# Optimization experiments

Measured on AMD Instinct MI355X. Metric: run time of the kernel, lower is better.

## Reference

```python
import jax, jax.numpy as jnp
import numpy as np

EPS = 1e-12


def conv3(x, W, b):
    # x: [B,C,H,W], W: [O,I,3,3] -> SAME conv, stride 1
    y = jax.lax.conv_general_dilated(x, W, (1, 1), 'SAME',
                                     dimension_numbers=('NCHW', 'OIHW', 'NCHW'))
    return y + b[None, :, None, None]


def unfold3(x):
    # torch F.unfold(kernel=3, padding=1): [B,C,H,W] -> [B, C*9, H*W]
    B, C, H, W = x.shape
    xp = jnp.pad(x, ((0, 0), (0, 0), (1, 1), (1, 1)))
    patches = jnp.stack([xp[:, :, i:i + H, j:j + W]
                         for i in range(3) for j in range(3)], axis=2)  # [B,C,9,H,W]
    return patches.reshape(B, C * 9, H * W)


def fold3(u, H, W):
    # torch F.fold(kernel=3, padding=1): [B, C*9, H*W] -> [B,C,H,W] (overlap-add)
    B = u.shape[0]
    C = u.shape[1] // 9
    p = u.reshape(B, C, 3, 3, H, W)
    out = jnp.zeros((B, C, H + 2, W + 2), u.dtype)
    for i in range(3):
        for j in range(3):
            out = out.at[:, :, i:i + H, j:j + W].add(p[:, :, i, j])
    return out[:, :, 1:-1, 1:-1]


def l2norm(v, axis):
    n = jnp.sqrt(jnp.sum(v * v, axis=axis, keepdims=True))
    return v / jnp.maximum(n, EPS)


def setup_inputs() -> dict:
    key = jax.random.key(0)
    ks = jax.random.split(key, 10)
    in_c, q_c = 64, 32
    B, H, W = 1, 96, 96
    s = 0.05
    return {
        'x':  jax.random.normal(ks[0], (B, in_c, H, W), jnp.float32),
        'W1': jax.random.normal(ks[1], (in_c, in_c, 3, 3), jnp.float32) * s,
        'b1': jax.random.normal(ks[2], (in_c,), jnp.float32) * s,
        'W2': jax.random.normal(ks[3], (in_c, in_c, 3, 3), jnp.float32) * s,
        'b2': jax.random.normal(ks[4], (in_c,), jnp.float32) * s,
        'Wq': jax.random.normal(ks[5], (q_c, in_c, 3, 3), jnp.float32) * s,
        'bq': jax.random.normal(ks[6], (q_c,), jnp.float32) * s,
        'Wk': jax.random.normal(ks[7], (q_c, in_c, 3, 3), jnp.float32) * s,
        'bk': jax.random.normal(ks[8], (q_c,), jnp.float32) * s,
    }


def reference(x, W1, b1, W2, b2, Wq, bq, Wk, bk):
    TOPK = 5
    B, C, H, W = x.shape
    L = H * W

    feature = jax.nn.relu(conv3(jax.nn.relu(conv3(x, W1, b1)), W2, b2))
    q = conv3(x, Wq, bq)
    k = conv3(x, Wk, bk)

    q_unfold = l2norm(unfold3(q), axis=1)                      # [B, Q9, L]
    k_unfold = l2norm(jnp.swapaxes(unfold3(k), 1, 2), axis=2)  # [B, L, Q9]

    R_qk = jnp.einsum('blc,bcm->blm', k_unfold, q_unfold)      # [B, L_k, L_q]

    # topk over dim=1 (key positions) for each query position
    vals, idxs = jax.lax.top_k(jnp.swapaxes(R_qk, 1, 2), TOPK)  # [B, L_q, K]
    R_maxs = jnp.swapaxes(vals, 1, 2)                           # [B, K, L]
    R_indexs = jnp.swapaxes(idxs, 1, 2)                         # [B, K, L]

    x_unfold = unfold3(x)                                       # [B, C*9, L]
    acc = jnp.zeros_like(x)
    for i in range(1, TOPK):
        idx = R_indexs[:, i, :][:, None, :]                     # [B,1,L]
        T_unfold = jnp.take_along_axis(x_unfold, idx, axis=2)   # [B, C*9, L]
        T = fold3(T_unfold, H, W) / 9.0
        S = R_maxs[:, i, :].reshape(B, 1, H, W)
        acc = acc + T * S
    y = feature + x + acc / float(TOPK - 1)
    return y
```

## Files before the change

### kernel.cpp

```cpp
#include <hip/hip_runtime.h>
#include <math.h>

#define HH 96
#define WW 96
#define LL 9216
#define PW 98
#define PCH (PW * PW)
#define D9 288
#define TOPK 5
#define NK 6
#define NCAND 8
#define KSPLIT 32
#define CPQ (KSPLIT * NK)
#define KEYS_PER_SPLIT (LL / KSPLIT)
#define PASSES (KEYS_PER_SPLIT / 32)
#define CHUNKS (32 * 36)
#define KROW 292

typedef short short8 __attribute__((ext_vector_type(8)));
typedef float f32x16 __attribute__((ext_vector_type(16)));

__device__ __forceinline__ float  asf(unsigned u) { union { unsigned u; float f; } a; a.u = u; return a.f; }
__device__ __forceinline__ unsigned asu(float f)  { union { float f; unsigned u; } a; a.f = f; return a.u; }

__device__ __forceinline__ unsigned short f2bf(float f) {
    unsigned u = asu(f);
    unsigned r = u + 0x7fff + ((u >> 16) & 1);
    return (unsigned short)(r >> 16);
}

template<int N>
__device__ __forceinline__ void ins_med3(float* v, float x) {
    float nv[N];
    nv[0] = fmaxf(v[0], x);
    #pragma unroll
    for (int s = 1; s < N; ++s) nv[s] = __builtin_amdgcn_fmed3f(v[s-1], v[s], x);
    #pragma unroll
    for (int s = 0; s < N; ++s) v[s] = nv[s];
}

__device__ __forceinline__ bool better_tb(float av, int ai, float bv, int bi) {
    return (av > bv) || (av == bv && ai < bi);
}

template<int N>
__device__ __forceinline__ void insert_tb(float (&v)[N], int (&ix)[N], float nv, int ni) {
    if (better_tb(nv, ni, v[N-1], ix[N-1])) {
        v[N-1] = nv; ix[N-1] = ni;
        #pragma unroll
        for (int s = N-1; s > 0; --s) {
            if (better_tb(v[s], ix[s], v[s-1], ix[s-1])) {
                float tv = v[s]; v[s] = v[s-1]; v[s-1] = tv;
                int ti = ix[s]; ix[s] = ix[s-1]; ix[s-1] = ti;
            }
        }
    }
}

__global__ __launch_bounds__(256) void pad_init_kernel(
    const float* __restrict__ x, float* __restrict__ xpad, float* __restrict__ c1pad)
{
    int e = blockIdx.x * 256 + threadIdx.x;
    if (blockIdx.y == 1) { c1pad[e] = 0.0f; return; }
    int c = e / PCH, rem = e - c * PCH;
    int r = rem / PW, col = rem - r * PW;
    float val = 0.0f;
    if ((unsigned)(r - 1) < 96u && (unsigned)(col - 1) < 96u)
        val = x[(size_t)c * LL + (r - 1) * WW + (col - 1)];
    xpad[e] = val;
}

template<int NCO>
__device__ __forceinline__ void conv_pipe(
    const float* __restrict__ inpad, const float* __restrict__ Wt,
    const float* __restrict__ bias, int co0,
    float (&acc)[NCO][2])
{
    int t = blockIdx.x * 256 + threadIdx.x;
    int pix0 = t * 2;
    int y = pix0 / WW, x0 = pix0 - y * WW;
    const float* base = inpad + y * PW + x0;

    #pragma unroll
    for (int j = 0; j < NCO; ++j) acc[j][0] = acc[j][1] = bias[co0 + j];

    float2 A[3][2], B[3][2];
    #pragma unroll
    for (int u = 0; u < 3; ++u) {
        A[u][0] = *(const float2*)(base + u * PW);
        A[u][1] = *(const float2*)(base + u * PW + 2);
    }

    #pragma unroll 1
    for (int ci = 0; ci < 64; ci += 2) {
        const float* nb = base + (size_t)(ci + 1) * PCH;
        #pragma unroll
        for (int u = 0; u < 3; ++u) {
            B[u][0] = *(const float2*)(nb + u * PW);
            B[u][1] = *(const float2*)(nb + u * PW + 2);
        }
        {
            const float* wb = Wt + ((size_t)co0 * 64 + ci) * 9;
            #pragma unroll
            for (int j = 0; j < NCO; ++j) {
                const float* wp = wb + (size_t)j * 64 * 9;
                #pragma unroll
                for (int u = 0; u < 3; ++u) {
                    float r0 = A[u][0].x, r1 = A[u][0].y, r2 = A[u][1].x, r3 = A[u][1].y;
                    float w0 = wp[u*3], w1 = wp[u*3+1], w2 = wp[u*3+2];
                    acc[j][0] = fmaf(r0, w0, acc[j][0]);
                    acc[j][1] = fmaf(r1, w0, acc[j][1]);
                    acc[j][0] = fmaf(r1, w1, acc[j][0]);
                    acc[j][1] = fmaf(r2, w1, acc[j][1]);
                    acc[j][0] = fmaf(r2, w2, acc[j][0]);
                    acc[j][1] = fmaf(r3, w2, acc[j][1]);
                }
            }
        }
        if (ci + 2 < 64) {
            const float* nb2 = base + (size_t)(ci + 2) * PCH;
            #pragma unroll
            for (int u = 0; u < 3; ++u) {
                A[u][0] = *(const float2*)(nb2 + u * PW);
                A[u][1] = *(const float2*)(nb2 + u * PW + 2);
            }
        }
        {
            const float* wb = Wt + ((size_t)co0 * 64 + (ci + 1)) * 9;
            #pragma unroll
            for (int j = 0; j < NCO; ++j) {
                const float* wp = wb + (size_t)j * 64 * 9;
                #pragma unroll
                for (int u = 0; u < 3; ++u) {
                    float r0 = B[u][0].x, r1 = B[u][0].y, r2 = B[u][1].x, r3 = B[u][1].y;
                    float w0 = wp[u*3], w1 = wp[u*3+1], w2 = wp[u*3+2];
                    acc[j][0] = fmaf(r0, w0, acc[j][0]);
                    acc[j][1] = fmaf(r1, w0, acc[j][1]);
                    acc[j][0] = fmaf(r1, w1, acc[j][0]);
                    acc[j][1] = fmaf(r2, w1, acc[j][1]);
                    acc[j][0] = fmaf(r2, w2, acc[j][0]);
                    acc[j][1] = fmaf(r3, w2, acc[j][1]);
                }
            }
        }
    }
}

__global__ __launch_bounds__(256) void conv_stage1_kernel(
    const float* __restrict__ xpad,
    const float* __restrict__ W1, const float* __restrict__ b1, float* __restrict__ c1pad,
    const float* __restrict__ Wq, const float* __restrict__ bq,
    const float* __restrict__ Wk, const float* __restrict__ bk,
    float* __restrict__ qq, float* __restrict__ kk)
{
    int g = blockIdx.y;
    int pix0 = (blockIdx.x * 256 + threadIdx.x) * 2;
    int y = pix0 / WW, x0 = pix0 - y * WW;

    if (g < 16) {
        float acc[4][2];
        conv_pipe<4>(xpad, W1, b1, g * 4, acc);
        #pragma unroll
        for (int j = 0; j < 4; ++j) {
            float* o = c1pad + (size_t)(g * 4 + j) * PCH + (y + 1) * PW + (x0 + 1);
            o[0] = fmaxf(acc[j][0], 0.0f);
            o[1] = fmaxf(acc[j][1], 0.0f);
        }
    } else if (g < 24) {
        float acc[4][2];
        conv_pipe<4>(xpad, Wq, bq, (g - 16) * 4, acc);
        #pragma unroll
        for (int j = 0; j < 4; ++j)
            *(float2*)(qq + (size_t)((g - 16) * 4 + j) * LL + pix0) = make_float2(acc[j][0], acc[j][1]);
    } else {
        float acc[4][2];
        conv_pipe<4>(xpad, Wk, bk, (g - 24) * 4, acc);
        #pragma unroll
        for (int j = 0; j < 4; ++j)
            *(float2*)(kk + (size_t)((g - 24) * 4 + j) * LL + pix0) = make_float2(acc[j][0], acc[j][1]);
    }
}

__global__ __launch_bounds__(256) void conv2_kernel(
    const float* __restrict__ c1pad, const float* __restrict__ W2,
    const float* __restrict__ b2, float* __restrict__ feat)
{
    int pix0 = (blockIdx.x * 256 + threadIdx.x) * 2;
    float acc[2][2];
    conv_pipe<2>(c1pad, W2, b2, blockIdx.y * 2, acc);
    #pragma unroll
    for (int j = 0; j < 2; ++j) {
        float2 o;
        o.x = fmaxf(acc[j][0], 0.0f);
        o.y = fmaxf(acc[j][1], 0.0f);
        *(float2*)(feat + (size_t)(blockIdx.y * 2 + j) * LL + pix0) = o;
    }
}

__global__ __launch_bounds__(256) void transpose_x_kernel(
    const float* __restrict__ x, float* __restrict__ xT)
{
    __shared__ float t[64][65];
    int pix0 = blockIdx.x * 64;
    int lp = threadIdx.x & 63, cg = threadIdx.x >> 6;
    #pragma unroll
    for (int cc = 0; cc < 16; ++cc) {
        int c = cg * 16 + cc;
        t[c][lp] = x[(size_t)c * LL + pix0 + lp];
    }
    __syncthreads();
    #pragma unroll
    for (int pp = 0; pp < 16; ++pp) {
        int pl = cg * 16 + pp;
        xT[(size_t)(pix0 + pl) * 64 + lp] = t[lp][pl];
    }
}

__global__ __launch_bounds__(256) void unfold_norm_kernel(
    const float* __restrict__ qq, float* __restrict__ q_f32, unsigned short* __restrict__ q_bf,
    const float* __restrict__ kk, float* __restrict__ k_f32, unsigned short* __restrict__ k_bf)
{
    const float* in; float* o32; unsigned short* obf;
    if (blockIdx.y == 0) { in = qq; o32 = q_f32; obf = q_bf; }
    else                 { in = kk; o32 = k_f32; obf = k_bf; }

    __shared__ float tile[3][32][34];
    __shared__ float inv_s[32];
    int tid = threadIdx.x;
    int l0 = blockIdx.x * 32;
    int y = l0 / WW, xb = l0 % WW;

    #pragma unroll
    for (int j = 0; j < 13; ++j) {
        int f = j * 256 + tid;
        if (f < 3 * 32 * 34) {
            int col = f % 34, cc = (f / 34) & 31, r = f / (34 * 32);
            int yy = y + r - 1, xv = xb + col - 1;
            float val = ((unsigned)yy < 96u && (unsigned)xv < 96u)
                        ? in[(size_t)cc * LL + yy * 96 + xv] : 0.0f;
            tile[r][cc][col] = val;
        }
    }
    __syncthreads();

    {
        int pxl = tid >> 3, sub = tid & 7;
        float ss = 0.0f;
        #pragma unroll
        for (int cc = 0; cc < 4; ++cc) {
            int c = sub * 4 + cc;
            #pragma unroll
            for (int u = 0; u < 3; ++u)
                #pragma unroll
                for (int v = 0; v < 3; ++v) {
                    float val = tile[u][c][pxl + v];
                    ss = fmaf(val, val, ss);
                }
        }
        ss += __shfl_xor(ss, 1);
        ss += __shfl_xor(ss, 2);
        ss += __shfl_xor(ss, 4);
        if (sub == 0) inv_s[pxl] = 1.0f / fmaxf(sqrtf(ss), 1e-12f);
    }
    __syncthreads();

    #pragma unroll 1
    for (int it = 0; it < 9; ++it) {
        int e = it * 256 + tid;
        int pxl = e / 72, dc = e - pxl * 72;
        int l = l0 + pxl;
        float inv = inv_s[pxl];
        float4 o; float* op = &o.x;
        #pragma unroll
        for (int i = 0; i < 4; ++i) {
            int d = dc * 4 + i;
            int c = d / 9, rm = d - c * 9;
            int u = rm / 3, v = rm - u * 3;
            op[i] = tile[u][c][pxl + v] * inv;
        }
        *(float4*)(o32 + (size_t)l * D9 + dc * 4) = o;
        unsigned short b4[4];
        #pragma unroll
        for (int i = 0; i < 4; ++i) b4[i] = f2bf(op[i]);
        *(uint2*)(obf + (size_t)l * D9 + dc * 4) = *(uint2*)b4;
    }
}

__global__ __launch_bounds__(256, 3) void topk_mfma_kernel(
    const unsigned short* __restrict__ qn_bf, const unsigned short* __restrict__ kn_bf,
    float* __restrict__ valsQ)
{
    __shared__ unsigned short ks[2][32 * KROW];

    int tid  = threadIdx.x;
    int lane = tid & 63;
    int col = lane & 31, khalf = lane >> 5;
    int qtile = blockIdx.x >> 5;
    int split = blockIdx.x & 31;
    int q0w = qtile * 128 + (tid >> 6) * 32;
    int key0 = split * KEYS_PER_SPLIT;

    short8 qf[18];
    {
        const unsigned short* qrow = qn_bf + (size_t)(q0w + col) * D9 + khalf * 8;
        #pragma unroll
        for (int dg = 0; dg < 18; ++dg)
            qf[dg] = *(const short8*)(qrow + dg * 16);
    }

    float lv[NK];
    #pragma unroll
    for (int s = 0; s < NK; ++s) lv[s] = -INFINITY;

    const char* kg = (const char*)kn_bf;
    uint4 pre[5];

    #pragma unroll
    for (int c0 = 0; c0 < 5; ++c0) {
        int c = tid + c0 * 256;
        if (c < CHUNKS) {
            int key = c / 36, off = c - key * 36;
            pre[c0] = *(const uint4*)(kg + (size_t)(key0 + key) * 576 + off * 16);
        }
    }
    #pragma unroll
    for (int c0 = 0; c0 < 5; ++c0) {
        int c = tid + c0 * 256;
        if (c < CHUNKS) {
            int key = c / 36, off = c - key * 36;
            char* d = (char*)ks[0] + key * (KROW*2) + off * 16;
            *(uint2*)d       = *(uint2*)&pre[c0];
            *(uint2*)(d + 8) = *((uint2*)&pre[c0] + 1);
        }
    }
    __syncthreads();

    for (int p = 0; p < PASSES; ++p) {
        if (p + 1 < PASSES) {
            #pragma unroll
            for (int c0 = 0; c0 < 5; ++c0) {
                int c = tid + c0 * 256;
                if (c < CHUNKS) {
                    int key = c / 36, off = c - key * 36;
                    pre[c0] = *(const uint4*)(kg + (size_t)(key0 + (p+1)*32 + key) * 576 + off * 16);
                }
            }
        }

        f32x16 acc = {};
        const char* kb = (const char*)ks[p & 1] + (size_t)col * (KROW*2) + khalf * 16;
        #pragma unroll
        for (int dg = 0; dg < 18; ++dg) {
            short8 af;
            *(uint2*)&af       = *(const uint2*)(kb + dg * 32);
            *((uint2*)&af + 1) = *(const uint2*)(kb + dg * 32 + 8);
            acc = __builtin_amdgcn_mfma_f32_32x32x16_bf16(af, qf[dg], acc, 0, 0, 0);
        }

        int lbase = p * 32 + 4 * khalf;
        #pragma unroll
        for (int r = 0; r < 16; ++r) {
            unsigned lkey = (unsigned)(lbase + (r & 3) + 8 * (r >> 2));
            ins_med3<NK>(lv, asf((asu(acc[r]) & 0xFFFFFE00u) | lkey));
        }

        if (p + 1 < PASSES) {
            #pragma unroll
            for (int c0 = 0; c0 < 5; ++c0) {
                int c = tid + c0 * 256;
                if (c < CHUNKS) {
                    int key = c / 36, off = c - key * 36;
                    char* d = (char*)ks[(p+1) & 1] + key * (KROW*2) + off * 16;
                    *(uint2*)d       = *(uint2*)&pre[c0];
                    *(uint2*)(d + 8) = *((uint2*)&pre[c0] + 1);
                }
            }
        }
        __syncthreads();
    }

    {
        float pv[NK];
        #pragma unroll
        for (int s = 0; s < NK; ++s) pv[s] = __shfl_xor(lv[s], 32);
        #pragma unroll
        for (int s = 0; s < NK; ++s) ins_med3<NK>(lv, pv[s]);
        if (lane < 32) {
            int q = q0w + col;
            float* vq = valsQ + (size_t)q * CPQ + split * NK;
            #pragma unroll
            for (int s = 0; s < NK; ++s) vq[s] = lv[s];
        }
    }
}

__global__ __launch_bounds__(256) void rerank_kernel(
    const float* __restrict__ valsQ,
    const float* __restrict__ qn_f32, const float* __restrict__ kn_f32,
    float* __restrict__ vals, int* __restrict__ idxs)
{
    int tid = threadIdx.x;
    int lane = tid & 63;
    int half = lane >> 5, l32 = lane & 31;
    int q = blockIdx.x * 8 + (tid >> 6) * 2 + half;

    const float* vq = valsQ + (size_t)q * CPQ + l32 * NK;
    float v[NK];
    #pragma unroll
    for (int s = 0; s < NK; ++s) v[s] = vq[s];

    int ckey[NCAND];
    #pragma unroll
    for (int it = 0; it < NCAND; ++it) {
        float cv = v[0];
        int cl = l32;
        #pragma unroll
        for (int st = 1; st < 32; st <<= 1) {
            float ov = __shfl_xor(cv, st);
            int ol = __shfl_xor(cl, st);
            if (ov > cv || (ov == cv && ol < cl)) { cv = ov; cl = ol; }
        }
        ckey[it] = cl * KEYS_PER_SPLIT + (int)(asu(cv) & 0x1FFu);
        if (cl == l32) {
            #pragma unroll
            for (int s = 0; s < NK-1; ++s) v[s] = v[s+1];
            v[NK-1] = -INFINITY;
        }
    }

    int r = l32 >> 2, part = l32 & 3;
    const float4* qr = (const float4*)(qn_f32 + (size_t)q * D9) + part * 18;
    const float4* kr = (const float4*)(kn_f32 + (size_t)ckey[r] * D9) + part * 18;
    float s0 = 0.f, s1 = 0.f, s2 = 0.f, s3 = 0.f;
    #pragma unroll
    for (int i2 = 0; i2 < 18; ++i2) {
        float4 a = qr[i2], b = kr[i2];
        s0 = fmaf(a.x, b.x, s0); s1 = fmaf(a.y, b.y, s1);
        s2 = fmaf(a.z, b.z, s2); s3 = fmaf(a.w, b.w, s3);
    }
    float sc = (s0 + s1) + (s2 + s3);
    sc += __shfl_xor(sc, 1);
    sc += __shfl_xor(sc, 2);

    float bv[TOPK]; int bi[TOPK];
    #pragma unroll
    for (int s = 0; s < TOPK; ++s) { bv[s] = -INFINITY; bi[s] = 0x7fffffff; }
    #pragma unroll
    for (int cc = 0; cc < NCAND; ++cc) {
        float sv = __shfl(sc, half * 32 + cc * 4);
        insert_tb<TOPK>(bv, bi, sv, ckey[cc]);
    }
    if (l32 == 0) {
        #pragma unroll
        for (int s = 0; s < TOPK; ++s) {
            vals[(size_t)s * LL + q] = bv[s];
            idxs[(size_t)s * LL + q] = bi[s];
        }
    }
}

__global__ __launch_bounds__(256) void gather_out_kernel(
    const float* __restrict__ xT, const float* __restrict__ feat,
    const float* __restrict__ vals, const int* __restrict__ idxs,
    float* __restrict__ out)
{
    int wave = threadIdx.x >> 6, lane = threadIdx.x & 63;
    int pix = blockIdx.x * 4 + wave;
    int y = pix / WW, x0 = pix - y * WW;
    float acc = 0.0f;
    #pragma unroll 1
    for (int s = 1; s < TOPK; ++s) {
        float S = vals[(size_t)s * LL + pix] * (1.0f/9.0f);
        #pragma unroll
        for (int i = 0; i < 3; ++i) {
            int qy = y + 1 - i;
            #pragma unroll
            for (int j = 0; j < 3; ++j) {
                int qx = x0 + 1 - j;
                if ((unsigned)qy < 96u && (unsigned)qx < 96u) {
                    int l = idxs[(size_t)s * LL + qy * WW + qx];
                    int yl = l / WW, xl = l - yl * WW;
                    int sy = yl + i - 1, sx = xl + j - 1;
                    if ((unsigned)sy < 96u && (unsigned)sx < 96u)
                        acc = fmaf(S, xT[(size_t)(sy * WW + sx) * 64 + lane], acc);
                }
            }
        }
    }
    out[(size_t)lane * LL + pix] = feat[(size_t)lane * LL + pix]
                                 + xT[(size_t)pix * 64 + lane] + acc * 0.25f;
}

extern "C" void kernel_launch(void* const* d_in, const int* in_sizes, int n_in,
                              void* d_out, int out_size, void* d_ws, size_t ws_size,
                              hipStream_t stream)
{
    (void)in_sizes; (void)n_in; (void)out_size; (void)ws_size;
    const float* x  = (const float*)d_in[0];
    const float* W1 = (const float*)d_in[1];
    const float* b1 = (const float*)d_in[2];
    const float* W2 = (const float*)d_in[3];
    const float* b2 = (const float*)d_in[4];
    const float* Wq = (const float*)d_in[5];
    const float* bq = (const float*)d_in[6];
    const float* Wk = (const float*)d_in[7];
    const float* bk = (const float*)d_in[8];
    float* out = (float*)d_out;

    char* p = (char*)d_ws;
    float* xpad   = (float*)p;            p += (size_t)64 * PCH * 4;
    float* c1pad  = (float*)p;            p += (size_t)64 * PCH * 4;
    float* feat   = (float*)p;            p += (size_t)64 * LL * 4;
    float* xT     = (float*)p;            p += (size_t)64 * LL * 4;
    float* qq     = (float*)p;            p += (size_t)32 * LL * 4;
    float* kk     = (float*)p;            p += (size_t)32 * LL * 4;
    float* qn_f32 = (float*)p;            p += (size_t)LL * D9 * 4;
    float* kn_f32 = (float*)p;            p += (size_t)LL * D9 * 4;
    unsigned short* qn_bf = (unsigned short*)p;  p += (size_t)LL * D9 * 2;
    unsigned short* kn_bf = (unsigned short*)p;  p += (size_t)LL * D9 * 2;
    float* valsQ  = (float*)p;            p += (size_t)LL * CPQ * 4;
    float* vals   = (float*)p;            p += (size_t)TOPK * LL * 4;
    int*   idxs   = (int*)p;              p += (size_t)TOPK * LL * 4;

    pad_init_kernel<<<dim3(2401, 2), 256, 0, stream>>>(x, xpad, c1pad);
    conv_stage1_kernel<<<dim3(18, 32), 256, 0, stream>>>(xpad, W1, b1, c1pad, Wq, bq, Wk, bk, qq, kk);
    unfold_norm_kernel<<<dim3(288, 2), 256, 0, stream>>>(qq, qn_f32, qn_bf, kk, kn_f32, kn_bf);
    topk_mfma_kernel<<<72 * KSPLIT, 256, 0, stream>>>(qn_bf, kn_bf, valsQ);
    conv2_kernel<<<dim3(18, 32), 256, 0, stream>>>(c1pad, W2, b2, feat);
    transpose_x_kernel<<<144, 256, 0, stream>>>(x, xT);
    rerank_kernel<<<LL / 8, 256, 0, stream>>>(valsQ, qn_f32, kn_f32, vals, idxs);
    gather_out_kernel<<<LL / 4, 256, 0, stream>>>(xT, feat, vals, idxs, out);
}
```

Before: 291.7 us.

## Store keys in MFMA fragment layout and merge topk, conv2, transpose launches

The key unfold kernel now writes bf16 keys directly in the MFMA A-fragment order, so each lane of the topk loop loads one contiguous 16-byte chunk from global memory and LDS instead of padded rows split into two 8-byte accesses. The topk, conv2 and x-transpose kernels are merged into one launch dispatched by block index, so the independent conv2 and transpose work can run alongside the topk blocks and two launches are removed. In exchange the conv2 and transpose blocks run under the topk kernel's launch bounds and shared-memory allocation, and the plain padded LDS layout may bring bank conflicts.

```diff
diff --git a/kernel.cpp b/kernel.cpp
--- a/kernel.cpp
+++ b/kernel.cpp
@@ -14,8 +14,11 @@
 #define CPQ (KSPLIT * NK)
 #define KEYS_PER_SPLIT (LL / KSPLIT)
 #define PASSES (KEYS_PER_SPLIT / 32)
-#define CHUNKS (32 * 36)
-#define KROW 292
+#define PCHUNK 1152
+
+#define TOPK_BLOCKS 2304
+#define CONV2_BLOCKS 576
+#define TRANS_BLOCKS 144
 
 typedef short short8 __attribute__((ext_vector_type(8)));
 typedef float f32x16 __attribute__((ext_vector_type(16)));
@@ -73,11 +76,9 @@
 template<int NCO>
 __device__ __forceinline__ void conv_pipe(
     const float* __restrict__ inpad, const float* __restrict__ Wt,
-    const float* __restrict__ bias, int co0,
+    const float* __restrict__ bias, int co0, int pix0,
     float (&acc)[NCO][2])
 {
-    int t = blockIdx.x * 256 + threadIdx.x;
-    int pix0 = t * 2;
     int y = pix0 / WW, x0 = pix0 - y * WW;
     const float* base = inpad + y * PW + x0;
 
@@ -159,7 +160,7 @@
 
     if (g < 16) {
         float acc[4][2];
-        conv_pipe<4>(xpad, W1, b1, g * 4, acc);
+        conv_pipe<4>(xpad, W1, b1, g * 4, pix0, acc);
         #pragma unroll
         for (int j = 0; j < 4; ++j) {
             float* o = c1pad + (size_t)(g * 4 + j) * PCH + (y + 1) * PW + (x0 + 1);
@@ -168,61 +169,26 @@
         }
     } else if (g < 24) {
         float acc[4][2];
-        conv_pipe<4>(xpad, Wq, bq, (g - 16) * 4, acc);
+        conv_pipe<4>(xpad, Wq, bq, (g - 16) * 4, pix0, acc);
         #pragma unroll
         for (int j = 0; j < 4; ++j)
             *(float2*)(qq + (size_t)((g - 16) * 4 + j) * LL + pix0) = make_float2(acc[j][0], acc[j][1]);
     } else {
         float acc[4][2];
-        conv_pipe<4>(xpad, Wk, bk, (g - 24) * 4, acc);
+        conv_pipe<4>(xpad, Wk, bk, (g - 24) * 4, pix0, acc);
         #pragma unroll
         for (int j = 0; j < 4; ++j)
             *(float2*)(kk + (size_t)((g - 24) * 4 + j) * LL + pix0) = make_float2(acc[j][0], acc[j][1]);
     }
 }
 
-__global__ __launch_bounds__(256) void conv2_kernel(
-    const float* __restrict__ c1pad, const float* __restrict__ W2,
-    const float* __restrict__ b2, float* __restrict__ feat)
-{
-    int pix0 = (blockIdx.x * 256 + threadIdx.x) * 2;
-    float acc[2][2];
-    conv_pipe<2>(c1pad, W2, b2, blockIdx.y * 2, acc);
-    #pragma unroll
-    for (int j = 0; j < 2; ++j) {
-        float2 o;
-        o.x = fmaxf(acc[j][0], 0.0f);
-        o.y = fmaxf(acc[j][1], 0.0f);
-        *(float2*)(feat + (size_t)(blockIdx.y * 2 + j) * LL + pix0) = o;
-    }
-}
-
-__global__ __launch_bounds__(256) void transpose_x_kernel(
-    const float* __restrict__ x, float* __restrict__ xT)
-{
-    __shared__ float t[64][65];
-    int pix0 = blockIdx.x * 64;
-    int lp = threadIdx.x & 63, cg = threadIdx.x >> 6;
-    #pragma unroll
-    for (int cc = 0; cc < 16; ++cc) {
-        int c = cg * 16 + cc;
-        t[c][lp] = x[(size_t)c * LL + pix0 + lp];
-    }
-    __syncthreads();
-    #pragma unroll
-    for (int pp = 0; pp < 16; ++pp) {
-        int pl = cg * 16 + pp;
-        xT[(size_t)(pix0 + pl) * 64 + lp] = t[lp][pl];
-    }
-}
-
 __global__ __launch_bounds__(256) void unfold_norm_kernel(
     const float* __restrict__ qq, float* __restrict__ q_f32, unsigned short* __restrict__ q_bf,
-    const float* __restrict__ kk, float* __restrict__ k_f32, unsigned short* __restrict__ k_bf)
-{
-    const float* in; float* o32; unsigned short* obf;
-    if (blockIdx.y == 0) { in = qq; o32 = q_f32; obf = q_bf; }
-    else                 { in = kk; o32 = k_f32; obf = k_bf; }
+    const float* __restrict__ kk, float* __restrict__ k_f32, short8* __restrict__ kn_afrag)
+{
+    int isK = blockIdx.y;
+    const float* in = isK ? kk : qq;
+    float* o32 = isK ? k_f32 : q_f32;
 
     __shared__ float tile[3][32][34];
     __shared__ float inv_s[32];
@@ -279,26 +245,45 @@
             op[i] = tile[u][c][pxl + v] * inv;
         }
         *(float4*)(o32 + (size_t)l * D9 + dc * 4) = o;
-        unsigned short b4[4];
-        #pragma unroll
-        for (int i = 0; i < 4; ++i) b4[i] = f2bf(op[i]);
-        *(uint2*)(obf + (size_t)l * D9 + dc * 4) = *(uint2*)b4;
-    }
-}
-
-__global__ __launch_bounds__(256, 3) void topk_mfma_kernel(
-    const unsigned short* __restrict__ qn_bf, const unsigned short* __restrict__ kn_bf,
-    float* __restrict__ valsQ)
-{
-    __shared__ unsigned short ks[2][32 * KROW];
-
-    int tid  = threadIdx.x;
+        if (!isK) {
+            unsigned short b4[4];
+            #pragma unroll
+            for (int i = 0; i < 4; ++i) b4[i] = f2bf(op[i]);
+            *(uint2*)(q_bf + (size_t)l * D9 + dc * 4) = *(uint2*)b4;
+        }
+    }
+
+    if (isK) {
+        #pragma unroll 1
+        for (int it = 0; it < 5; ++it) {
+            int e = it * 256 + tid;
+            if (e < 1152) {
+                int j = e >> 5, pxl = e & 31;
+                int dg = j >> 1, half = j & 1;
+                float inv = inv_s[pxl];
+                unsigned short b8[8];
+                #pragma unroll
+                for (int i = 0; i < 8; ++i) {
+                    int d = dg * 16 + half * 8 + i;
+                    int c = d / 9, rm = d - c * 9;
+                    int u = rm / 3, v = rm - u * 3;
+                    b8[i] = f2bf(tile[u][c][pxl + v] * inv);
+                }
+                kn_afrag[(size_t)((blockIdx.x * 18 + dg) * 64 + half * 32 + pxl)] = *(short8*)b8;
+            }
+        }
+    }
+}
+
+__device__ __forceinline__ void topk_body(
+    int bx, int tid, const unsigned short* __restrict__ qn_bf,
+    const uint4* __restrict__ kn_afrag, float* __restrict__ valsQ, uint4* ks)
+{
     int lane = tid & 63;
     int col = lane & 31, khalf = lane >> 5;
-    int qtile = blockIdx.x >> 5;
-    int split = blockIdx.x & 31;
+    int qtile = bx >> 5;
+    int split = bx & 31;
     int q0w = qtile * 128 + (tid >> 6) * 32;
-    int key0 = split * KEYS_PER_SPLIT;
 
     short8 qf[18];
     {
@@ -312,26 +297,18 @@
     #pragma unroll
     for (int s = 0; s < NK; ++s) lv[s] = -INFINITY;
 
-    const char* kg = (const char*)kn_bf;
+    const uint4* afr = kn_afrag + (size_t)split * (PASSES * PCHUNK);
+
     uint4 pre[5];
-
     #pragma unroll
     for (int c0 = 0; c0 < 5; ++c0) {
         int c = tid + c0 * 256;
-        if (c < CHUNKS) {
-            int key = c / 36, off = c - key * 36;
-            pre[c0] = *(const uint4*)(kg + (size_t)(key0 + key) * 576 + off * 16);
-        }
+        if (c < PCHUNK) pre[c0] = afr[c];
     }
     #pragma unroll
     for (int c0 = 0; c0 < 5; ++c0) {
         int c = tid + c0 * 256;
-        if (c < CHUNKS) {
-            int key = c / 36, off = c - key * 36;
-            char* d = (char*)ks[0] + key * (KROW*2) + off * 16;
-            *(uint2*)d       = *(uint2*)&pre[c0];
-            *(uint2*)(d + 8) = *((uint2*)&pre[c0] + 1);
-        }
+        if (c < PCHUNK) ks[c] = pre[c0];
     }
     __syncthreads();
 
@@ -340,20 +317,17 @@
             #pragma unroll
             for (int c0 = 0; c0 < 5; ++c0) {
                 int c = tid + c0 * 256;
-                if (c < CHUNKS) {
-                    int key = c / 36, off = c - key * 36;
-                    pre[c0] = *(const uint4*)(kg + (size_t)(key0 + (p+1)*32 + key) * 576 + off * 16);
-                }
+                if (c < PCHUNK) pre[c0] = afr[(size_t)(p + 1) * PCHUNK + c];
             }
         }
 
         f32x16 acc = {};
-        const char* kb = (const char*)ks[p & 1] + (size_t)col * (KROW*2) + khalf * 16;
+        const uint4* kb = ks + (p & 1) * PCHUNK + lane;
         #pragma unroll
         for (int dg = 0; dg < 18; ++dg) {
+            uint4 t = kb[dg * 64];
             short8 af;
-            *(uint2*)&af       = *(const uint2*)(kb + dg * 32);
-            *((uint2*)&af + 1) = *(const uint2*)(kb + dg * 32 + 8);
+            *(uint4*)&af = t;
             acc = __builtin_amdgcn_mfma_f32_32x32x16_bf16(af, qf[dg], acc, 0, 0, 0);
         }
 
@@ -368,12 +342,7 @@
             #pragma unroll
             for (int c0 = 0; c0 < 5; ++c0) {
                 int c = tid + c0 * 256;
-                if (c < CHUNKS) {
-                    int key = c / 36, off = c - key * 36;
-                    char* d = (char*)ks[(p+1) & 1] + key * (KROW*2) + off * 16;
-                    *(uint2*)d       = *(uint2*)&pre[c0];
-                    *(uint2*)(d + 8) = *((uint2*)&pre[c0] + 1);
-                }
+                if (c < PCHUNK) ks[((p + 1) & 1) * PCHUNK + c] = pre[c0];
             }
         }
         __syncthreads();
@@ -390,6 +359,50 @@
             float* vq = valsQ + (size_t)q * CPQ + split * NK;
             #pragma unroll
             for (int s = 0; s < NK; ++s) vq[s] = lv[s];
+        }
+    }
+}
+
+__global__ __launch_bounds__(256, 3) void fused_main_kernel(
+    const unsigned short* __restrict__ qn_bf, const uint4* __restrict__ kn_afrag,
+    float* __restrict__ valsQ,
+    const float* __restrict__ c1pad, const float* __restrict__ W2,
+    const float* __restrict__ b2, float* __restrict__ feat,
+    const float* __restrict__ x, float* __restrict__ xT)
+{
+    __shared__ alignas(16) char smem[2 * PCHUNK * 16];
+    int bx = blockIdx.x, tid = threadIdx.x;
+
+    if (bx < TOPK_BLOCKS) {
+        topk_body(bx, tid, qn_bf, kn_afrag, valsQ, (uint4*)smem);
+    } else if (bx < TOPK_BLOCKS + CONV2_BLOCKS) {
+        int idx = bx - TOPK_BLOCKS;
+        int cx = idx % 18, cy = idx / 18;
+        int pix0 = (cx * 256 + tid) * 2;
+        float acc[2][2];
+        conv_pipe<2>(c1pad, W2, b2, cy * 2, pix0, acc);
+        #pragma unroll
+        for (int j = 0; j < 2; ++j) {
+            float2 o;
+            o.x = fmaxf(acc[j][0], 0.0f);
+            o.y = fmaxf(acc[j][1], 0.0f);
+            *(float2*)(feat + (size_t)(cy * 2 + j) * LL + pix0) = o;
+        }
+    } else {
+        int idx = bx - TOPK_BLOCKS - CONV2_BLOCKS;
+        float (*t)[65] = (float (*)[65])smem;
+        int pix0 = idx * 64;
+        int lp = tid & 63, cg = tid >> 6;
+        #pragma unroll
+        for (int cc = 0; cc < 16; ++cc) {
+            int c = cg * 16 + cc;
+            t[c][lp] = x[(size_t)c * LL + pix0 + lp];
+        }
+        __syncthreads();
+        #pragma unroll
+        for (int pp = 0; pp < 16; ++pp) {
+            int pl = cg * 16 + pp;
+            xT[(size_t)(pix0 + pl) * 64 + lp] = t[lp][pl];
         }
     }
 }
@@ -517,17 +530,16 @@
     float* qn_f32 = (float*)p;            p += (size_t)LL * D9 * 4;
     float* kn_f32 = (float*)p;            p += (size_t)LL * D9 * 4;
     unsigned short* qn_bf = (unsigned short*)p;  p += (size_t)LL * D9 * 2;
-    unsigned short* kn_bf = (unsigned short*)p;  p += (size_t)LL * D9 * 2;
+    short8* kn_afrag = (short8*)p;        p += (size_t)KSPLIT * PASSES * 18 * 64 * 16;
     float* valsQ  = (float*)p;            p += (size_t)LL * CPQ * 4;
     float* vals   = (float*)p;            p += (size_t)TOPK * LL * 4;
     int*   idxs   = (int*)p;              p += (size_t)TOPK * LL * 4;
 
     pad_init_kernel<<<dim3(2401, 2), 256, 0, stream>>>(x, xpad, c1pad);
     conv_stage1_kernel<<<dim3(18, 32), 256, 0, stream>>>(xpad, W1, b1, c1pad, Wq, bq, Wk, bk, qq, kk);
-    unfold_norm_kernel<<<dim3(288, 2), 256, 0, stream>>>(qq, qn_f32, qn_bf, kk, kn_f32, kn_bf);
-    topk_mfma_kernel<<<72 * KSPLIT, 256, 0, stream>>>(qn_bf, kn_bf, valsQ);
-    conv2_kernel<<<dim3(18, 32), 256, 0, stream>>>(c1pad, W2, b2, feat);
-    transpose_x_kernel<<<144, 256, 0, stream>>>(x, xT);
+    unfold_norm_kernel<<<dim3(288, 2), 256, 0, stream>>>(qq, qn_f32, qn_bf, kk, kn_f32, kn_afrag);
+    fused_main_kernel<<<TOPK_BLOCKS + CONV2_BLOCKS + TRANS_BLOCKS, 256, 0, stream>>>(
+        qn_bf, (const uint4*)kn_afrag, valsQ, c1pad, W2, b2, feat, x, xT);
     rerank_kernel<<<LL / 8, 256, 0, stream>>>(valsQ, qn_f32, kn_f32, vals, idxs);
     gather_out_kernel<<<LL / 4, 256, 0, stream>>>(xT, feat, vals, idxs, out);
 }
```

Result: slower. 332.6 us (+14.0%).
